# Kernel tuning notes

Hardware: AMD Instinct MI355X
Metric: run time of the kernel (lower is better)

Reference implementation:

```python
import jax, jax.numpy as jnp
import numpy as np

B, F, N, D = 4, 5, 2048, 256


def setup_inputs() -> dict:
    key = jax.random.key(0)
    k1, k2 = jax.random.split(key)
    x = jax.random.normal(k1, (B, F, N, D), dtype=jnp.float32)
    y = jax.random.normal(k2, (B, F, N, D), dtype=jnp.float32)
    return {"x": x, "y": y}


def _weight(a, b):
    # pairwise_distance with p=2 in the original is sum((a-b)**2)**(1/(2-1)),
    # i.e. SQUARED euclidean distance (no sqrt). Use gram expansion to avoid
    # materializing the [B,F,N,N,D] difference tensor.
    a2 = jnp.sum(a * a, axis=-1)                      # [B,F,N]
    b2 = jnp.sum(b * b, axis=-1)                      # [B,F,M]
    ab = jnp.einsum('bfnd,bfmd->bfnm', a, b)          # [B,F,N,M]
    d = a2[..., :, None] + b2[..., None, :] - 2.0 * ab  # squared dists
    # min over neighbors (dim=1 of the per-frame matrix), mean over query
    # nodes, then mean over frames -> one scalar per batch element.
    return jnp.mean(jnp.min(d, axis=-1), axis=(-1, -2))  # [B]


def _normalize(f):
    # min/max over the node dim (dim=2), per (batch, frame, feature)
    mn = jnp.min(f, axis=2, keepdims=True)
    mx = jnp.max(f, axis=2, keepdims=True)
    return (f - mn) / (mx - mn)


def reference(x, y):
    wx = 1.0 / (1.0 + _weight(x, y))  # [B]
    wy = 1.0 / (1.0 + _weight(y, x))  # [B]
    nx = _normalize(x)
    ny = _normalize(y)
    return wx[:, None, None, None] * nx + wy[:, None, None, None] * ny
```

## Files before the change

kernel.cpp:

```cpp
#include <hip/hip_runtime.h>

typedef unsigned int u32;
typedef unsigned short u16;
typedef __attribute__((ext_vector_type(8))) short short8;
typedef __attribute__((ext_vector_type(4))) float floatx4;

#define NB 4
#define NF 5
#define NN 2048
#define NDM 256
#define NBF (NB*NF)
#define NBFN (NBF*NN)
#define NBFD (NBF*NDM)

#define AS1 __attribute__((address_space(1)))
#define AS3 __attribute__((address_space(3)))

__device__ u16    g_xb[(size_t)NBF*NN*NDM];
__device__ u16    g_yb[(size_t)NBF*NN*NDM];
__device__ float  g_a2[NBFN];
__device__ float  g_b2[NBFN];
__device__ float  g_rpart[(size_t)4*NBFN];
__device__ float  g_cpart[(size_t)64*NBFN];
__device__ float  g_pmn[2][(size_t)32*NBFD];
__device__ float  g_pmx[2][(size_t)32*NBFD];
__device__ float  g_bfsum[2*NBF];
__device__ float4 g_coef[NBFD];

__device__ __forceinline__ u16 cvt_bf16(float f){
  u32 b = __float_as_uint(f);
  return (u16)((b + 0x7FFFu + ((b >> 16) & 1u)) >> 16);
}
__device__ __forceinline__ void load16(const void* g, void* l){
  __builtin_amdgcn_global_load_lds((AS1 const void*)g, (AS3 void*)l, 16, 0, 0);
}

__global__ void __launch_bounds__(256) k_prep(const float* __restrict__ x,
                                              const float* __restrict__ y){
  int bi = blockIdx.x;
  if (bi == 0 && threadIdx.x < 2*NBF) g_bfsum[threadIdx.x] = 0.f;
  int tensor = bi >= (NBF*32); int rem = bi - tensor*(NBF*32);
  int bf = rem >> 5; int chunk = rem & 31;
  size_t rbase = (size_t)bf*NN + (size_t)chunk*64;
  const float* src = (tensor ? y : x) + rbase*NDM;
  u16*  dst  = (tensor ? g_yb : g_xb) + rbase*NDM;
  float* sums = (tensor ? g_b2 : g_a2) + bf*NN + chunk*64;
  int w = threadIdx.x >> 6, l = threadIdx.x & 63;

  float4 vmn = make_float4(INFINITY,INFINITY,INFINITY,INFINITY);
  float4 vmx = make_float4(-INFINITY,-INFINITY,-INFINITY,-INFINITY);
  for (int i = 0; i < 16; ++i){
    int row = w + 4*i;
    float4 v = ((const float4*)(src + (size_t)row*NDM))[l];
    float s = v.x*v.x + v.y*v.y + v.z*v.z + v.w*v.w;
    #pragma unroll
    for (int m = 1; m < 64; m <<= 1) s += __shfl_xor(s, m, 64);
    ((ushort4*)(dst + (size_t)row*NDM))[l] =
        make_ushort4(cvt_bf16(v.x), cvt_bf16(v.y), cvt_bf16(v.z), cvt_bf16(v.w));
    if (l == 0) sums[row] = s;
    vmn.x = fminf(vmn.x, v.x); vmn.y = fminf(vmn.y, v.y);
    vmn.z = fminf(vmn.z, v.z); vmn.w = fminf(vmn.w, v.w);
    vmx.x = fmaxf(vmx.x, v.x); vmx.y = fmaxf(vmx.y, v.y);
    vmx.z = fmaxf(vmx.z, v.z); vmx.w = fmaxf(vmx.w, v.w);
  }
  __shared__ float4 smn[4][64], smx[4][64];
  smn[w][l] = vmn; smx[w][l] = vmx;
  __syncthreads();
  if (w == 0){
    float4 a = smn[0][l], b_ = smn[1][l], c = smn[2][l], d = smn[3][l];
    float4 e = smx[0][l], f = smx[1][l], g = smx[2][l], h = smx[3][l];
    float4 mn4 = make_float4(fminf(fminf(a.x,b_.x), fminf(c.x,d.x)),
                             fminf(fminf(a.y,b_.y), fminf(c.y,d.y)),
                             fminf(fminf(a.z,b_.z), fminf(c.z,d.z)),
                             fminf(fminf(a.w,b_.w), fminf(c.w,d.w)));
    float4 mx4 = make_float4(fmaxf(fmaxf(e.x,f.x), fmaxf(g.x,h.x)),
                             fmaxf(fmaxf(e.y,f.y), fmaxf(g.y,h.y)),
                             fmaxf(fmaxf(e.z,f.z), fmaxf(g.z,h.z)),
                             fmaxf(fmaxf(e.w,f.w), fmaxf(g.w,h.w)));
    ((float4*)&g_pmn[tensor][(size_t)chunk*NBFD + bf*NDM])[l] = mn4;
    ((float4*)&g_pmx[tensor][(size_t)chunk*NBFD + bf*NDM])[l] = mx4;
  }
}

__global__ void __launch_bounds__(256, 2) k_gemm(){
  __shared__ u16 Bs[2][128*64];
  const int bf = blockIdx.z;
  const int i0 = blockIdx.y * 128;
  const int jq = blockIdx.x;
  const int t = threadIdx.x;
  const int w = t >> 6, l = t & 63;
  const int quad = l >> 4, c16 = l & 15;
  const int wrow = w * 32;
  const u16* xb = g_xb + (size_t)bf * NN * NDM;
  const u16* yb = g_yb + (size_t)bf * NN * NDM;
  const int lr = l >> 3, gj = (l & 7) ^ lr;

  short8 af[2][8];
  #pragma unroll
  for (int mb = 0; mb < 2; ++mb){
    const u16* rp = xb + (size_t)(i0 + wrow + mb*16 + c16) * NDM + quad*8;
    #pragma unroll
    for (int ks = 0; ks < 8; ++ks)
      af[mb][ks] = *(const short8*)(rp + ks*32);
  }
  const float* a2 = g_a2 + bf*NN + i0 + wrow;
  const float* b2 = g_b2 + bf*NN;
  float a2r[2][4];
  #pragma unroll
  for (int mb = 0; mb < 2; ++mb)
    #pragma unroll
    for (int r = 0; r < 4; ++r)
      a2r[mb][r] = a2[mb*16 + quad*4 + r];

  float rm[2][4];
  #pragma unroll
  for (int mb = 0; mb < 2; ++mb)
    #pragma unroll
    for (int r = 0; r < 4; ++r) rm[mb][r] = INFINITY;

  auto stage = [&](int jt, int kc, int bb){
    const int j0 = jq*512 + jt*128;
    #pragma unroll
    for (int q = 0; q < 4; ++q){
      const int c = w*4 + q;
      const int r = c*8 + lr;
      load16(yb + (size_t)(j0 + r)*NDM + kc*64 + gj*8, &Bs[bb][c*512]);
    }
  };

  int buf = 0;
  stage(0, 0, 0);
  for (int jj = 0; jj < 4; ++jj){
    const int j0 = jq*512 + jj*128;
    floatx4 acc[2][8] = {};
    #pragma unroll
    for (int kc = 0; kc < 4; ++kc){
      __syncthreads();
      const int nit = jj*4 + kc + 1;
      if (nit < 16) stage(nit >> 2, nit & 3, buf ^ 1);
      #pragma unroll
      for (int kb = 0; kb < 2; ++kb){
        const int p8 = ((kb*4 + quad) ^ (c16 & 7)) * 8;
        short8 bq[8];
        #pragma unroll
        for (int nb = 0; nb < 8; ++nb)
          bq[nb] = *(const short8*)&Bs[buf][(nb*16 + c16)*64 + p8];
        #pragma unroll
        for (int mb = 0; mb < 2; ++mb)
          #pragma unroll
          for (int nb = 0; nb < 8; ++nb)
            acc[mb][nb] = __builtin_amdgcn_mfma_f32_16x16x32_bf16(af[mb][kc*2+kb], bq[nb], acc[mb][nb], 0, 0, 0);
      }
      buf ^= 1;
    }
    float bcol[8], colm[8];
    #pragma unroll
    for (int nb = 0; nb < 8; ++nb){
      bcol[nb] = b2[j0 + nb*16 + c16];
      colm[nb] = INFINITY;
    }
    #pragma unroll
    for (int mb = 0; mb < 2; ++mb)
      #pragma unroll
      for (int r = 0; r < 4; ++r)
        #pragma unroll
        for (int nb = 0; nb < 8; ++nb){
          float dd = a2r[mb][r] + bcol[nb] - 2.0f * acc[mb][nb][r];
          rm[mb][r] = fminf(rm[mb][r], dd);
          colm[nb] = fminf(colm[nb], dd);
        }
    #pragma unroll
    for (int nb = 0; nb < 8; ++nb){
      float cm = colm[nb];
      cm = fminf(cm, __shfl_xor(cm, 16, 64));
      cm = fminf(cm, __shfl_xor(cm, 32, 64));
      if (quad == 0)
        g_cpart[(size_t)(blockIdx.y*4 + w)*NBFN + bf*NN + j0 + nb*16 + c16] = cm;
    }
  }
  #pragma unroll
  for (int mb = 0; mb < 2; ++mb)
    #pragma unroll
    for (int r = 0; r < 4; ++r){
      float v = rm[mb][r];
      v = fminf(v, __shfl_xor(v, 1, 64));
      v = fminf(v, __shfl_xor(v, 2, 64));
      v = fminf(v, __shfl_xor(v, 4, 64));
      v = fminf(v, __shfl_xor(v, 8, 64));
      if (c16 == 0)
        g_rpart[(size_t)jq*NBFN + bf*NN + i0 + wrow + mb*16 + quad*4 + r] = v;
    }
}

__global__ void __launch_bounds__(256) k_weight(){
  int bf = blockIdx.x >> 3;
  int chunk = blockIdx.x & 7;
  int i = chunk*256 + threadIdx.x;
  size_t base = (size_t)bf*NN + i;
  float m = INFINITY, c = INFINITY;
  #pragma unroll
  for (int p = 0; p < 4; ++p)  m = fminf(m, g_rpart[(size_t)p*NBFN + base]);
  #pragma unroll
  for (int p = 0; p < 64; ++p) c = fminf(c, g_cpart[(size_t)p*NBFN + base]);
  float srow = m, scol = c;
  #pragma unroll
  for (int mm = 1; mm < 64; mm <<= 1){
    srow += __shfl_xor(srow, mm, 64);
    scol += __shfl_xor(scol, mm, 64);
  }
  __shared__ float pr[4], pcn[4];
  int w = threadIdx.x >> 6, l = threadIdx.x & 63;
  if (l == 0){ pr[w] = srow; pcn[w] = scol; }
  __syncthreads();
  if (threadIdx.x == 0){
    atomicAdd(&g_bfsum[bf],       pr[0]+pr[1]+pr[2]+pr[3]);
    atomicAdd(&g_bfsum[NBF + bf], pcn[0]+pcn[1]+pcn[2]+pcn[3]);
  }
}

__global__ void k_coef(){
  int idx = blockIdx.x * 256 + threadIdx.x;
  int bf = idx >> 8;
  int b = bf / NF;
  float swx = 0.f, swy = 0.f;
  #pragma unroll
  for (int f = 0; f < NF; ++f){
    swx += g_bfsum[b*NF + f];
    swy += g_bfsum[NBF + b*NF + f];
  }
  float wx = 1.0f / (1.0f + swx * (1.0f/(NF*NN)));
  float wy = 1.0f / (1.0f + swy * (1.0f/(NF*NN)));
  float mnx = INFINITY, mxx = -INFINITY, mny = INFINITY, mxy = -INFINITY;
  #pragma unroll
  for (int c = 0; c < 32; ++c){
    mnx = fminf(mnx, g_pmn[0][(size_t)c*NBFD + idx]);
    mxx = fmaxf(mxx, g_pmx[0][(size_t)c*NBFD + idx]);
    mny = fminf(mny, g_pmn[1][(size_t)c*NBFD + idx]);
    mxy = fmaxf(mxy, g_pmx[1][(size_t)c*NBFD + idx]);
  }
  float sx = wx / (mxx - mnx), sy = wy / (mxy - mny);
  g_coef[idx] = make_float4(sx, -sx * mnx, sy, -sy * mny);
}

__global__ void __launch_bounds__(256) k_out(const float4* __restrict__ x,
                                             const float4* __restrict__ y,
                                             floatx4* __restrict__ out){
  size_t i = (size_t)blockIdx.x * 256 + threadIdx.x;
  float4 xv = x[i], yv = y[i];
  size_t base = i * 4;
  int bf = (int)(base >> 19);
  int d0 = (int)(base & 255);
  const float4* cf = &g_coef[bf * 256 + d0];
  float4 c0 = cf[0], c1 = cf[1], c2 = cf[2], c3 = cf[3];
  floatx4 o;
  o.x = c0.x * xv.x + c0.y + c0.z * yv.x + c0.w;
  o.y = c1.x * xv.y + c1.y + c1.z * yv.y + c1.w;
  o.z = c2.x * xv.z + c2.y + c2.z * yv.z + c2.w;
  o.w = c3.x * xv.w + c3.y + c3.z * yv.w + c3.w;
  __builtin_nontemporal_store(o, &out[i]);
}

extern "C" void kernel_launch(void* const* d_in, const int* in_sizes, int n_in,
                              void* d_out, int out_size, void* d_ws, size_t ws_size,
                              hipStream_t stream) {
  const float* x = (const float*)d_in[0];
  const float* y = (const float*)d_in[1];
  (void)d_ws; (void)ws_size; (void)in_sizes; (void)n_in; (void)out_size;

  k_prep  <<<dim3(1280),       dim3(256), 0, stream>>>(x, y);
  k_gemm  <<<dim3(4, 16, 20),  dim3(256), 0, stream>>>();
  k_weight<<<dim3(160),        dim3(256), 0, stream>>>();
  k_coef  <<<dim3(20),         dim3(256), 0, stream>>>();
  k_out   <<<dim3(10240),      dim3(256), 0, stream>>>((const float4*)x, (const float4*)y,
                                                       (floatx4*)d_out);
}
```

Before: 218.5 us.

## Stage wider K-slices in GEMM, cache b2 in LDS, loop k_out per block

The GEMM kernel now stages 128-wide K slices of Y per barrier instead of 64, using a new XOR swizzle. This halves the number of __syncthreads and staging rounds but doubles LDS use per block, which may limit occupancy. The b2 column norms are preloaded into shared memory once per block rather than read from global memory at each epilogue. The output kernel now uses 320 blocks that each loop over 128 rows, so the coefficients are loaded once per thread instead of once per element.

```diff
diff --git a/kernel.cpp b/kernel.cpp
--- a/kernel.cpp
+++ b/kernel.cpp
@@ -83,7 +83,8 @@
 }
 
 __global__ void __launch_bounds__(256, 2) k_gemm(){
-  __shared__ u16 Bs[2][128*64];
+  __shared__ u16 Bs[2][128*128];
+  __shared__ float b2s[512];
   const int bf = blockIdx.z;
   const int i0 = blockIdx.y * 128;
   const int jq = blockIdx.x;
@@ -93,7 +94,9 @@
   const int wrow = w * 32;
   const u16* xb = g_xb + (size_t)bf * NN * NDM;
   const u16* yb = g_yb + (size_t)bf * NN * NDM;
-  const int lr = l >> 3, gj = (l & 7) ^ lr;
+
+  const float* b2 = g_b2 + bf*NN;
+  ((float2*)b2s)[t] = ((const float2*)(b2 + jq*512))[t];
 
   short8 af[2][8];
   #pragma unroll
@@ -104,7 +107,6 @@
       af[mb][ks] = *(const short8*)(rp + ks*32);
   }
   const float* a2 = g_a2 + bf*NN + i0 + wrow;
-  const float* b2 = g_b2 + bf*NN;
   float a2r[2][4];
   #pragma unroll
   for (int mb = 0; mb < 2; ++mb)
@@ -118,13 +120,14 @@
     #pragma unroll
     for (int r = 0; r < 4; ++r) rm[mb][r] = INFINITY;
 
-  auto stage = [&](int jt, int kc, int bb){
+  auto stage = [&](int jt, int h, int bb){
     const int j0 = jq*512 + jt*128;
     #pragma unroll
-    for (int q = 0; q < 4; ++q){
-      const int c = w*4 + q;
-      const int r = c*8 + lr;
-      load16(yb + (size_t)(j0 + r)*NDM + kc*64 + gj*8, &Bs[bb][c*512]);
+    for (int q = 0; q < 8; ++q){
+      const int row = q*16 + w*4 + (l >> 4);
+      const int c = (l & 15) ^ (row & 15);
+      load16(yb + (size_t)(j0 + row)*NDM + h*128 + c*8,
+             &Bs[bb][(q*16 + w*4)*128]);
     }
   };
 
@@ -134,29 +137,29 @@
     const int j0 = jq*512 + jj*128;
     floatx4 acc[2][8] = {};
     #pragma unroll
-    for (int kc = 0; kc < 4; ++kc){
+    for (int h = 0; h < 2; ++h){
       __syncthreads();
-      const int nit = jj*4 + kc + 1;
-      if (nit < 16) stage(nit >> 2, nit & 3, buf ^ 1);
+      const int nit = jj*2 + h + 1;
+      if (nit < 8) stage(nit >> 1, nit & 1, buf ^ 1);
       #pragma unroll
-      for (int kb = 0; kb < 2; ++kb){
-        const int p8 = ((kb*4 + quad) ^ (c16 & 7)) * 8;
+      for (int ksl = 0; ksl < 4; ++ksl){
+        const int lc = ((ksl*4 + quad) ^ c16) * 8;
         short8 bq[8];
         #pragma unroll
         for (int nb = 0; nb < 8; ++nb)
-          bq[nb] = *(const short8*)&Bs[buf][(nb*16 + c16)*64 + p8];
+          bq[nb] = *(const short8*)&Bs[buf][(nb*16 + c16)*128 + lc];
         #pragma unroll
         for (int mb = 0; mb < 2; ++mb)
           #pragma unroll
           for (int nb = 0; nb < 8; ++nb)
-            acc[mb][nb] = __builtin_amdgcn_mfma_f32_16x16x32_bf16(af[mb][kc*2+kb], bq[nb], acc[mb][nb], 0, 0, 0);
+            acc[mb][nb] = __builtin_amdgcn_mfma_f32_16x16x32_bf16(af[mb][h*4+ksl], bq[nb], acc[mb][nb], 0, 0, 0);
       }
       buf ^= 1;
     }
     float bcol[8], colm[8];
     #pragma unroll
     for (int nb = 0; nb < 8; ++nb){
-      bcol[nb] = b2[j0 + nb*16 + c16];
+      bcol[nb] = b2s[jj*128 + nb*16 + c16];
       colm[nb] = INFINITY;
     }
     #pragma unroll
@@ -245,19 +248,24 @@
 __global__ void __launch_bounds__(256) k_out(const float4* __restrict__ x,
                                              const float4* __restrict__ y,
                                              floatx4* __restrict__ out){
-  size_t i = (size_t)blockIdx.x * 256 + threadIdx.x;
-  float4 xv = x[i], yv = y[i];
-  size_t base = i * 4;
-  int bf = (int)(base >> 19);
-  int d0 = (int)(base & 255);
-  const float4* cf = &g_coef[bf * 256 + d0];
-  float4 c0 = cf[0], c1 = cf[1], c2 = cf[2], c3 = cf[3];
-  floatx4 o;
-  o.x = c0.x * xv.x + c0.y + c0.z * yv.x + c0.w;
-  o.y = c1.x * xv.y + c1.y + c1.z * yv.y + c1.w;
-  o.z = c2.x * xv.z + c2.y + c2.z * yv.z + c2.w;
-  o.w = c3.x * xv.w + c3.y + c3.z * yv.w + c3.w;
-  __builtin_nontemporal_store(o, &out[i]);
+  const int bf = blockIdx.x >> 4;
+  const int chunk = blockIdx.x & 15;
+  const int d4 = threadIdx.x & 63;
+  const int rsub = threadIdx.x >> 6;
+  const float4* cf = &g_coef[bf*256 + d4*4];
+  const float4 c0 = cf[0], c1 = cf[1], c2 = cf[2], c3 = cf[3];
+  const size_t base = ((size_t)bf*NN + chunk*128) * 64 + d4;
+  #pragma unroll 4
+  for (int it = 0; it < 32; ++it){
+    size_t idx = base + (size_t)(it*4 + rsub) * 64;
+    float4 xv = x[idx], yv = y[idx];
+    floatx4 o;
+    o.x = c0.x * xv.x + c0.y + c0.z * yv.x + c0.w;
+    o.y = c1.x * xv.y + c1.y + c1.z * yv.y + c1.w;
+    o.z = c2.x * xv.z + c2.y + c2.z * yv.z + c2.w;
+    o.w = c3.x * xv.w + c3.y + c3.z * yv.w + c3.w;
+    __builtin_nontemporal_store(o, &out[idx]);
+  }
 }
 
 extern "C" void kernel_launch(void* const* d_in, const int* in_sizes, int n_in,
@@ -267,10 +275,10 @@
   const float* y = (const float*)d_in[1];
   (void)d_ws; (void)ws_size; (void)in_sizes; (void)n_in; (void)out_size;
 
-  k_prep  <<<dim3(1280),       dim3(256), 0, stream>>>(x, y);
-  k_gemm  <<<dim3(4, 16, 20),  dim3(256), 0, stream>>>();
-  k_weight<<<dim3(160),        dim3(256), 0, stream>>>();
-  k_coef  <<<dim3(20),         dim3(256), 0, stream>>>();
-  k_out   <<<dim3(10240),      dim3(256), 0, stream>>>((const float4*)x, (const float4*)y,
-                                                       (floatx4*)d_out);
-}
+  k_prep  <<<dim3(1280),      dim3(256), 0, stream>>>(x, y);
+  k_gemm  <<<dim3(4, 16, 20), dim3(256), 0, stream>>>();
+  k_weight<<<dim3(160),       dim3(256), 0, stream>>>();
+  k_coef  <<<dim3(20),        dim3(256), 0, stream>>>();
+  k_out   <<<dim3(320),       dim3(256), 0, stream>>>((const float4*)x, (const float4*)y,
+                                                      (floatx4*)d_out);
+}
```

Result: no change. 217.9 us (-0.3%).
